# Kernel optimization log

Hardware: AMD Instinct MI355X
Metric: run time of the kernel (lower is better)

## Reference

```python
import jax, jax.numpy as jnp
import numpy as np

HEADS = 8
DIM_HEAD = 64
SCALE = DIM_HEAD ** -0.5


def setup_inputs() -> dict:
    key = jax.random.key(0)
    ks = jax.random.split(key, 7)
    b, n, m = 2, 4096, 4096
    query_dim, context_dim, inner = 1024, 768, HEADS * DIM_HEAD
    s = 0.02
    return {
        "x": jax.random.normal(ks[0], (b, n, query_dim), jnp.float32),
        "context": jax.random.normal(ks[1], (b, m, context_dim), jnp.float32),
        "Wq": jax.random.normal(ks[2], (query_dim, inner), jnp.float32) * s,
        "Wk": jax.random.normal(ks[3], (context_dim, inner), jnp.float32) * s,
        "Wv": jax.random.normal(ks[4], (context_dim, inner), jnp.float32) * s,
        "Wo": jax.random.normal(ks[5], (inner, query_dim), jnp.float32) * s,
        "bo": jnp.zeros((query_dim,), jnp.float32),
    }


def reference(x, context, Wq, Wk, Wv, Wo, bo):
    b, n, _ = x.shape
    m = context.shape[1]
    # projections (no bias), split heads: b n (h d) -> b n h d
    q = (x @ Wq).reshape(b, n, HEADS, DIM_HEAD)
    k = (context @ Wk).reshape(b, m, HEADS, DIM_HEAD)
    v = (context @ Wv).reshape(b, m, HEADS, DIM_HEAD)
    # fp32 QK^T (ATTN_PRECISION='fp32' path), full [b,h,n,m] scores
    sim = jnp.einsum("bihd,bjhd->bhij", q.astype(jnp.float32), k.astype(jnp.float32)) * SCALE
    attn = jax.nn.softmax(sim, axis=-1).astype(v.dtype)
    out = jnp.einsum("bhij,bjhd->bihd", attn, v).reshape(b, n, HEADS * DIM_HEAD)
    # to_out: Linear with bias (dropout=0 is identity)
    return out @ Wo + bo
```

## Files before the change

### kernel.cpp

```cpp
#include <hip/hip_runtime.h>
#include <hip/hip_bf16.h>
#include <cmath>


using bf16_t = __hip_bfloat16;
typedef __bf16 bf16x8 __attribute__((ext_vector_type(8)));
typedef float  f32x4  __attribute__((ext_vector_type(4)));

static constexpr int BATCH = 2;
static constexpr int NQ    = 4096;
static constexpr int NKV   = 4096;
static constexpr int NH    = 8;
static constexpr int DH    = 64;
static constexpr int INNER = NH * DH;
static constexpr int QDIM  = 1024;
static constexpr int CDIM  = 768;
static constexpr float QSCALE = 0.125f * 1.4426950408889634f;

#define MFMA_BF16(a, b, c) __builtin_amdgcn_mfma_f32_16x16x32_bf16((a), (b), (c), 0, 0, 0)

__device__ __forceinline__ float fast_exp2(float x) {
  return __builtin_amdgcn_exp2f(x);
}

__device__ __forceinline__ void gload_lds16(const bf16_t* g, bf16_t* l) {
  __builtin_amdgcn_global_load_lds(
      (const __attribute__((address_space(1))) unsigned int*)(uintptr_t)g,
      (__attribute__((address_space(3))) unsigned int*)(unsigned int)(uintptr_t)l,
      16, 0, 0);
}

__global__ __launch_bounds__(256) void cast_kernel(const float* __restrict__ in,
                                                   bf16_t* __restrict__ out, int n8) {
  int id = blockIdx.x * 256 + threadIdx.x;
  if (id >= n8) return;
  float4 a = ((const float4*)in)[2 * id];
  float4 b = ((const float4*)in)[2 * id + 1];
  bf16_t t[8] = {__float2bfloat16(a.x), __float2bfloat16(a.y), __float2bfloat16(a.z),
                 __float2bfloat16(a.w), __float2bfloat16(b.x), __float2bfloat16(b.y),
                 __float2bfloat16(b.z), __float2bfloat16(b.w)};
  ((uint4*)out)[id] = *(const uint4*)t;
}

__global__ __launch_bounds__(256) void wtrans_kernel(const float* __restrict__ W,
                                                     bf16_t* __restrict__ WT,
                                                     int K, int N) {
  __shared__ float tile[32][33];
  const int bn = blockIdx.x * 32, bk = blockIdx.y * 32;
  const int tx = threadIdx.x & 31, ty = threadIdx.x >> 5;
  for (int yy = ty; yy < 32; yy += 8)
    tile[yy][tx] = W[(size_t)(bk + yy) * N + bn + tx];
  __syncthreads();
  for (int yy = ty; yy < 32; yy += 8)
    WT[(size_t)(bn + yy) * K + bk + tx] = __float2bfloat16(tile[tx][yy]);
}

template <int IM, int OUT_MODE>
__global__ __launch_bounds__(256) void gemm_kernel(const bf16_t* __restrict__ A,
                                                   const bf16_t* __restrict__ WT,
                                                   void* __restrict__ Cp,
                                                   void* __restrict__ Cp2,
                                                   const float* __restrict__ bias,
                                                   float ascale, int M, int N, int K) {
  constexpr int BM = IM * 32;
  __shared__ __align__(16) bf16_t As[BM][32];
  __shared__ __align__(16) bf16_t Bs[128][32];
  const int tid = threadIdx.x;
  const int lane = tid & 63, wave = tid >> 6;
  const int lane15 = lane & 15, quad = lane >> 4;
  const int wm = (wave >> 1) * (BM / 2), wn = (wave & 1) * 64;
  const int m0 = blockIdx.x * BM, n0 = blockIdx.y * 128;

  const f32x4 vzero = {0.f, 0.f, 0.f, 0.f};
  f32x4 acc[IM][4];
  for (int i = 0; i < IM; ++i)
    for (int j = 0; j < 4; ++j) acc[i][j] = vzero;

  const int crow = lane >> 2, ccol = (lane & 3) * 8;
  for (int k0 = 0; k0 < K; k0 += 32) {
    if constexpr (IM == 4) {
      for (int cc = 0; cc < 2; ++cc) {
        int c = wave * 2 + cc;
        gload_lds16(A + (size_t)(m0 + c * 16 + crow) * K + k0 + ccol, &As[c * 16][0]);
        gload_lds16(WT + (size_t)(n0 + c * 16 + crow) * K + k0 + ccol, &Bs[c * 16][0]);
      }
    } else {
      gload_lds16(A + (size_t)(m0 + wave * 16 + crow) * K + k0 + ccol, &As[wave * 16][0]);
      for (int cc = 0; cc < 2; ++cc) {
        int c = wave * 2 + cc;
        gload_lds16(WT + (size_t)(n0 + c * 16 + crow) * K + k0 + ccol, &Bs[c * 16][0]);
      }
    }
    __syncthreads();
    bf16x8 af[IM], bfr[4];
    for (int i = 0; i < IM; ++i)
      af[i] = *reinterpret_cast<const bf16x8*>(&As[wm + i * 16 + lane15][quad * 8]);
    for (int j = 0; j < 4; ++j)
      bfr[j] = *reinterpret_cast<const bf16x8*>(&Bs[wn + j * 16 + lane15][quad * 8]);
    for (int i = 0; i < IM; ++i)
      for (int j = 0; j < 4; ++j) acc[i][j] = MFMA_BF16(af[i], bfr[j], acc[i][j]);
    __syncthreads();
  }

  for (int i = 0; i < IM; ++i) {
    int gm = m0 + wm + i * 16 + quad * 4;
    for (int j = 0; j < 4; ++j) {
      int gn = n0 + wn + j * 16 + lane15;
      for (int r = 0; r < 4; ++r) {
        float v = acc[i][j][r];
        if constexpr (OUT_MODE == 0) {
          ((bf16_t*)Cp)[(size_t)(gm + r) * N + gn] = __float2bfloat16(v * ascale);
        } else if constexpr (OUT_MODE == 1) {
          ((float*)Cp)[(size_t)(gm + r) * N + gn] = v + bias[gn];
        } else {
          if (gn < INNER) {
            ((bf16_t*)Cp)[(size_t)(gm + r) * INNER + gn] = __float2bfloat16(v);
          } else {
            int gmr = gm + r;
            ((bf16_t*)Cp2)[((size_t)(gmr >> 12) * INNER + (gn - INNER)) * (size_t)NKV +
                           (gmr & 4095)] = __float2bfloat16(v);
          }
        }
      }
    }
  }
}

__global__ __launch_bounds__(512) void attn_kernel(const bf16_t* Qg ,
                                                   const bf16_t* __restrict__ Kg ,
                                                   const bf16_t* __restrict__ Vtg ,
                                                   bf16_t* Og ) {
  __shared__ __align__(16) bf16_t KsF[2][8][512];
  __shared__ __align__(16) bf16_t VtF[2][8][512];
  __shared__ __align__(16) bf16_t PsA[128][72];

  const int tid = threadIdx.x;
  const int lane = tid & 63, wave = tid >> 6;
  const int lane15 = lane & 15, quad = lane >> 4;
  const int wrow = wave * 16;
  const int q0 = blockIdx.x * 128;
  const int h = blockIdx.y;
  const int b = blockIdx.z;

  const size_t qbase  = ((size_t)b * NQ + q0) * INNER + h * DH;
  const size_t kbase  = ((size_t)b * NKV) * INNER + h * DH;
  const size_t vtbase = ((size_t)(b * NH + h) * DH) * NKV;

  bf16x8 qf[2];
  for (int ks = 0; ks < 2; ++ks)
    qf[ks] = *reinterpret_cast<const bf16x8*>(
        Qg + qbase + (size_t)(wrow + lane15) * INNER + ks * 32 + quad * 8);

  const f32x4 vzero = {0.f, 0.f, 0.f, 0.f};
  f32x4 acc_o[4];
  float l_part = 0.f;
  for (int j = 0; j < 4; ++j) acc_o[j] = vzero;

  const int cw = wave;
  auto kaddr = [&](int kv0) {
    return Kg + kbase + (size_t)(kv0 + (cw & 3) * 16 + lane15) * INNER + (cw >> 2) * 32 + quad * 8;
  };
  auto vaddr = [&](int kv0) {
    return Vtg + vtbase + (size_t)((cw & 3) * 16 + lane15) * NKV + kv0 + (cw >> 2) * 32 + quad * 8;
  };
  uint4 kr = *(const uint4*)kaddr(0);
  uint4 vr = *(const uint4*)vaddr(0);

  constexpr int T = NKV / 64;
  for (int t = 0; t < T; ++t) {
    const int cur = t & 1;
    *(uint4*)&KsF[cur][cw][lane * 8] = kr;
    *(uint4*)&VtF[cur][cw][lane * 8] = vr;
    __syncthreads();

    f32x4 acc_st[4];
    for (int j = 0; j < 4; ++j) acc_st[j] = vzero;
    for (int ks = 0; ks < 2; ++ks) {
      bf16x8 kf[4];
      for (int j = 0; j < 4; ++j)
        kf[j] = *reinterpret_cast<const bf16x8*>(&KsF[cur][ks * 4 + j][lane * 8]);
      for (int j = 0; j < 4; ++j) acc_st[j] = MFMA_BF16(kf[j], qf[ks], acc_st[j]);
    }

    if (t + 1 < T) {
      int kv0n = (t + 1) * 64;
      kr = *(const uint4*)kaddr(kv0n);
      vr = *(const uint4*)vaddr(kv0n);
    }

    for (int j = 0; j < 4; ++j) {
      bf16_t t4[4];
      for (int r = 0; r < 4; ++r) {
        float p = fast_exp2(acc_st[j][r]);
        l_part += p;
        t4[r] = __float2bfloat16(p);
      }
      *(uint2*)&PsA[wrow + lane15][j * 16 + quad * 4] = *(const uint2*)t4;
    }
    __syncthreads();

    for (int ks = 0; ks < 2; ++ks) {
      bf16x8 pf, vf[4];
      pf = *reinterpret_cast<const bf16x8*>(&PsA[wrow + lane15][ks * 32 + quad * 8]);
      for (int j = 0; j < 4; ++j)
        vf[j] = *reinterpret_cast<const bf16x8*>(&VtF[cur][ks * 4 + j][lane * 8]);
      for (int j = 0; j < 4; ++j) acc_o[j] = MFMA_BF16(pf, vf[j], acc_o[j]);
    }
  }

  float l = l_part;
  l += __shfl_xor(l, 16, 64);
  l += __shfl_xor(l, 32, 64);
  float inv = 1.f / l;
  for (int r = 0; r < 4; ++r) {
    float invr = __shfl(inv, quad * 4 + r, 16);
    int row = wrow + quad * 4 + r;
    for (int j = 0; j < 4; ++j)
      Og[qbase + (size_t)row * INNER + j * 16 + lane15] =
          __float2bfloat16(acc_o[j][r] * invr);
  }
}

extern "C" void kernel_launch(void* const* d_in, const int* in_sizes, int n_in,
                              void* d_out, int out_size, void* d_ws, size_t ws_size,
                              hipStream_t stream) {
  (void)in_sizes; (void)n_in; (void)out_size; (void)ws_size;
  const float* x   = (const float*)d_in[0];
  const float* ctx = (const float*)d_in[1];
  const float* Wq  = (const float*)d_in[2];
  const float* Wk  = (const float*)d_in[3];
  const float* Wv  = (const float*)d_in[4];
  const float* Wo  = (const float*)d_in[5];
  const float* bo  = (const float*)d_in[6];
  float* out = (float*)d_out;

  char* ws = (char*)d_ws;
  size_t off = 0;
  auto take = [&](size_t nelem) { bf16_t* p = (bf16_t*)(ws + off); off += nelem * 2; return p; };
  bf16_t* WqT  = take((size_t)INNER * QDIM);
  bf16_t* WkvT = take((size_t)(2 * INNER) * CDIM);
  bf16_t* WoT  = take((size_t)QDIM * INNER);
  bf16_t* qob  = take((size_t)BATCH * NQ * INNER);
  bf16_t* kb   = take((size_t)BATCH * NKV * INNER);
  bf16_t* vtb  = take((size_t)BATCH * INNER * NKV);

  bf16_t* xb   = (bf16_t*)d_out;
  bf16_t* ctxb = xb + (size_t)BATCH * NQ * QDIM;

  const int M = BATCH * NQ;
  const int xN8 = BATCH * NQ * QDIM / 8, cN8 = BATCH * NKV * CDIM / 8;

  cast_kernel<<<(xN8 + 255) / 256, 256, 0, stream>>>(x, xb, xN8);
  cast_kernel<<<(cN8 + 255) / 256, 256, 0, stream>>>(ctx, ctxb, cN8);
  wtrans_kernel<<<dim3(INNER / 32, QDIM / 32), 256, 0, stream>>>(Wq, WqT, QDIM, INNER);
  wtrans_kernel<<<dim3(INNER / 32, CDIM / 32), 256, 0, stream>>>(Wk, WkvT, CDIM, INNER);
  wtrans_kernel<<<dim3(INNER / 32, CDIM / 32), 256, 0, stream>>>(
      Wv, WkvT + (size_t)INNER * CDIM, CDIM, INNER);
  wtrans_kernel<<<dim3(QDIM / 32, INNER / 32), 256, 0, stream>>>(Wo, WoT, INNER, QDIM);

  gemm_kernel<2, 0><<<dim3(M / 64, INNER / 128), 256, 0, stream>>>(
      xb, WqT, qob, nullptr, nullptr, QSCALE, M, INNER, QDIM);
  gemm_kernel<2, 3><<<dim3(M / 64, (2 * INNER) / 128), 256, 0, stream>>>(
      ctxb, WkvT, kb, vtb, nullptr, 1.f, M, 2 * INNER, CDIM);

  attn_kernel<<<dim3(NQ / 128, NH, BATCH), 512, 0, stream>>>(qob, kb, vtb, qob);

  gemm_kernel<2, 1><<<dim3(M / 64, QDIM / 128), 256, 0, stream>>>(
      qob, WoT, out, nullptr, bo, 1.f, M, QDIM, INNER);
}
```

Before: 280.4 us.

## Merge prep launches, double-buffer GEMM tiles, relax attention P barrier

Folds the two input cast launches into one kernel and the four weight-transpose launches into one 3D-grid kernel, cutting launch count. The GEMM drops direct global-to-LDS loads in favour of register prefetch of the next K slice into a double-buffered LDS tile, which removes one block barrier per iteration. In the attention inner loop, the block-wide barrier after writing the P tile becomes an LDS wait count. That relies on each wave reading only the P rows it wrote itself, so ordering against other waves is no longer enforced.

```diff
diff --git a/kernel.cpp b/kernel.cpp
--- a/kernel.cpp
+++ b/kernel.cpp
@@ -23,17 +23,20 @@
   return __builtin_amdgcn_exp2f(x);
 }
 
-__device__ __forceinline__ void gload_lds16(const bf16_t* g, bf16_t* l) {
-  __builtin_amdgcn_global_load_lds(
-      (const __attribute__((address_space(1))) unsigned int*)(uintptr_t)g,
-      (__attribute__((address_space(3))) unsigned int*)(unsigned int)(uintptr_t)l,
-      16, 0, 0);
-}
-
-__global__ __launch_bounds__(256) void cast_kernel(const float* __restrict__ in,
-                                                   bf16_t* __restrict__ out, int n8) {
+__global__ __launch_bounds__(256) void cast2_kernel(const float* __restrict__ x,
+                                                    bf16_t* __restrict__ xb, int xn8,
+                                                    const float* __restrict__ c,
+                                                    bf16_t* __restrict__ cb, int cn8) {
   int id = blockIdx.x * 256 + threadIdx.x;
-  if (id >= n8) return;
+  const float* in;
+  bf16_t* out;
+  if (id < xn8) {
+    in = x; out = xb;
+  } else {
+    id -= xn8;
+    if (id >= cn8) return;
+    in = c; out = cb;
+  }
   float4 a = ((const float4*)in)[2 * id];
   float4 b = ((const float4*)in)[2 * id + 1];
   bf16_t t[8] = {__float2bfloat16(a.x), __float2bfloat16(a.y), __float2bfloat16(a.z),
@@ -42,11 +45,25 @@
   ((uint4*)out)[id] = *(const uint4*)t;
 }
 
-__global__ __launch_bounds__(256) void wtrans_kernel(const float* __restrict__ W,
-                                                     bf16_t* __restrict__ WT,
-                                                     int K, int N) {
+__global__ __launch_bounds__(256) void wtrans4_kernel(const float* __restrict__ Wq,
+                                                      const float* __restrict__ Wk,
+                                                      const float* __restrict__ Wv,
+                                                      const float* __restrict__ Wo,
+                                                      bf16_t* __restrict__ WqT,
+                                                      bf16_t* __restrict__ WkvT,
+                                                      bf16_t* __restrict__ WoT) {
   __shared__ float tile[32][33];
+  const float* W;
+  bf16_t* WT;
+  int K, N;
+  switch (blockIdx.z) {
+    case 0: W = Wq; WT = WqT; K = QDIM; N = INNER; break;
+    case 1: W = Wk; WT = WkvT; K = CDIM; N = INNER; break;
+    case 2: W = Wv; WT = WkvT + (size_t)INNER * CDIM; K = CDIM; N = INNER; break;
+    default: W = Wo; WT = WoT; K = INNER; N = QDIM; break;
+  }
   const int bn = blockIdx.x * 32, bk = blockIdx.y * 32;
+  if (bn >= N || bk >= K) return;
   const int tx = threadIdx.x & 31, ty = threadIdx.x >> 5;
   for (int yy = ty; yy < 32; yy += 8)
     tile[yy][tx] = W[(size_t)(bk + yy) * N + bn + tx];
@@ -55,54 +72,57 @@
     WT[(size_t)(bn + yy) * K + bk + tx] = __float2bfloat16(tile[tx][yy]);
 }
 
-template <int IM, int OUT_MODE>
+template <int OUT_MODE>
 __global__ __launch_bounds__(256) void gemm_kernel(const bf16_t* __restrict__ A,
                                                    const bf16_t* __restrict__ WT,
                                                    void* __restrict__ Cp,
                                                    void* __restrict__ Cp2,
                                                    const float* __restrict__ bias,
                                                    float ascale, int M, int N, int K) {
-  constexpr int BM = IM * 32;
-  __shared__ __align__(16) bf16_t As[BM][32];
-  __shared__ __align__(16) bf16_t Bs[128][32];
+  __shared__ __align__(16) bf16_t As[2][64][32];
+  __shared__ __align__(16) bf16_t Bs[2][128][32];
   const int tid = threadIdx.x;
   const int lane = tid & 63, wave = tid >> 6;
   const int lane15 = lane & 15, quad = lane >> 4;
-  const int wm = (wave >> 1) * (BM / 2), wn = (wave & 1) * 64;
-  const int m0 = blockIdx.x * BM, n0 = blockIdx.y * 128;
+  const int wm = (wave >> 1) * 32, wn = (wave & 1) * 64;
+  const int m0 = blockIdx.x * 64, n0 = blockIdx.y * 128;
 
   const f32x4 vzero = {0.f, 0.f, 0.f, 0.f};
-  f32x4 acc[IM][4];
-  for (int i = 0; i < IM; ++i)
+  f32x4 acc[2][4];
+  for (int i = 0; i < 2; ++i)
     for (int j = 0; j < 4; ++j) acc[i][j] = vzero;
 
-  const int crow = lane >> 2, ccol = (lane & 3) * 8;
-  for (int k0 = 0; k0 < K; k0 += 32) {
-    if constexpr (IM == 4) {
-      for (int cc = 0; cc < 2; ++cc) {
-        int c = wave * 2 + cc;
-        gload_lds16(A + (size_t)(m0 + c * 16 + crow) * K + k0 + ccol, &As[c * 16][0]);
-        gload_lds16(WT + (size_t)(n0 + c * 16 + crow) * K + k0 + ccol, &Bs[c * 16][0]);
-      }
-    } else {
-      gload_lds16(A + (size_t)(m0 + wave * 16 + crow) * K + k0 + ccol, &As[wave * 16][0]);
-      for (int cc = 0; cc < 2; ++cc) {
-        int c = wave * 2 + cc;
-        gload_lds16(WT + (size_t)(n0 + c * 16 + crow) * K + k0 + ccol, &Bs[c * 16][0]);
-      }
-    }
+  const int srow = tid >> 2, sc8 = (tid & 3) * 8;
+  const bf16_t* aptr  = A + (size_t)(m0 + srow) * K + sc8;
+  const bf16_t* bptr0 = WT + (size_t)(n0 + srow) * K + sc8;
+  const bf16_t* bptr1 = WT + (size_t)(n0 + srow + 64) * K + sc8;
+  uint4 ar = *(const uint4*)aptr;
+  uint4 br0 = *(const uint4*)bptr0;
+  uint4 br1 = *(const uint4*)bptr1;
+
+  const int T = K / 32;
+  for (int t = 0; t < T; ++t) {
+    const int cur = t & 1;
+    *(uint4*)&As[cur][srow][sc8]      = ar;
+    *(uint4*)&Bs[cur][srow][sc8]      = br0;
+    *(uint4*)&Bs[cur][srow + 64][sc8] = br1;
     __syncthreads();
-    bf16x8 af[IM], bfr[4];
-    for (int i = 0; i < IM; ++i)
-      af[i] = *reinterpret_cast<const bf16x8*>(&As[wm + i * 16 + lane15][quad * 8]);
+    if (t + 1 < T) {
+      aptr += 32; bptr0 += 32; bptr1 += 32;
+      ar  = *(const uint4*)aptr;
+      br0 = *(const uint4*)bptr0;
+      br1 = *(const uint4*)bptr1;
+    }
+    bf16x8 af[2], bfr[4];
+    for (int i = 0; i < 2; ++i)
+      af[i] = *reinterpret_cast<const bf16x8*>(&As[cur][wm + i * 16 + lane15][quad * 8]);
     for (int j = 0; j < 4; ++j)
-      bfr[j] = *reinterpret_cast<const bf16x8*>(&Bs[wn + j * 16 + lane15][quad * 8]);
-    for (int i = 0; i < IM; ++i)
+      bfr[j] = *reinterpret_cast<const bf16x8*>(&Bs[cur][wn + j * 16 + lane15][quad * 8]);
+    for (int i = 0; i < 2; ++i)
       for (int j = 0; j < 4; ++j) acc[i][j] = MFMA_BF16(af[i], bfr[j], acc[i][j]);
-    __syncthreads();
-  }
-
-  for (int i = 0; i < IM; ++i) {
+  }
+
+  for (int i = 0; i < 2; ++i) {
     int gm = m0 + wm + i * 16 + quad * 4;
     for (int j = 0; j < 4; ++j) {
       int gn = n0 + wn + j * 16 + lane15;
@@ -197,7 +217,7 @@
       }
       *(uint2*)&PsA[wrow + lane15][j * 16 + quad * 4] = *(const uint2*)t4;
     }
-    __syncthreads();
+    asm volatile("s_waitcnt lgkmcnt(0)" ::: "memory");
 
     for (int ks = 0; ks < 2; ++ks) {
       bf16x8 pf, vf[4];
@@ -250,21 +270,16 @@
   const int M = BATCH * NQ;
   const int xN8 = BATCH * NQ * QDIM / 8, cN8 = BATCH * NKV * CDIM / 8;
 
-  cast_kernel<<<(xN8 + 255) / 256, 256, 0, stream>>>(x, xb, xN8);
-  cast_kernel<<<(cN8 + 255) / 256, 256, 0, stream>>>(ctx, ctxb, cN8);
-  wtrans_kernel<<<dim3(INNER / 32, QDIM / 32), 256, 0, stream>>>(Wq, WqT, QDIM, INNER);
-  wtrans_kernel<<<dim3(INNER / 32, CDIM / 32), 256, 0, stream>>>(Wk, WkvT, CDIM, INNER);
-  wtrans_kernel<<<dim3(INNER / 32, CDIM / 32), 256, 0, stream>>>(
-      Wv, WkvT + (size_t)INNER * CDIM, CDIM, INNER);
-  wtrans_kernel<<<dim3(QDIM / 32, INNER / 32), 256, 0, stream>>>(Wo, WoT, INNER, QDIM);
-
-  gemm_kernel<2, 0><<<dim3(M / 64, INNER / 128), 256, 0, stream>>>(
+  cast2_kernel<<<(xN8 + cN8 + 255) / 256, 256, 0, stream>>>(x, xb, xN8, ctx, ctxb, cN8);
+  wtrans4_kernel<<<dim3(32, 32, 4), 256, 0, stream>>>(Wq, Wk, Wv, Wo, WqT, WkvT, WoT);
+
+  gemm_kernel<0><<<dim3(M / 64, INNER / 128), 256, 0, stream>>>(
       xb, WqT, qob, nullptr, nullptr, QSCALE, M, INNER, QDIM);
-  gemm_kernel<2, 3><<<dim3(M / 64, (2 * INNER) / 128), 256, 0, stream>>>(
+  gemm_kernel<3><<<dim3(M / 64, (2 * INNER) / 128), 256, 0, stream>>>(
       ctxb, WkvT, kb, vtb, nullptr, 1.f, M, 2 * INNER, CDIM);
 
   attn_kernel<<<dim3(NQ / 128, NH, BATCH), 512, 0, stream>>>(qob, kb, vtb, qob);
 
-  gemm_kernel<2, 1><<<dim3(M / 64, QDIM / 128), 256, 0, stream>>>(
+  gemm_kernel<1><<<dim3(M / 64, QDIM / 128), 256, 0, stream>>>(
       qob, WoT, out, nullptr, bo, 1.f, M, QDIM, INNER);
 }
```

After: 266.0 us. 1.05x faster.
